# Performance work log

Hardware: AMD Instinct MI355X
Metric: run time of the kernel (lower is better)

## Reference

```python
import jax, jax.numpy as jnp
import numpy as np
import math

SAMPLE_RATIO = 0.25
K = 5
EPS = 1e-6

def _cells(loc_orig, H, W):
    # map normalized [-1,1] coords to nearest grid cell index, as in tcformer token2map/map2token
    loc = jnp.clip(loc_orig, -1.0, 1.0)
    px = jnp.clip(jnp.round(0.5 * (loc[..., 0] + 1.0) * W - 0.5).astype(jnp.int32), 0, W - 1)
    py = jnp.clip(jnp.round(0.5 * (loc[..., 1] + 1.0) * H - 0.5).astype(jnp.int32), 0, H - 1)
    return py * W + px  # [B, N0]

def token2map(x, loc_orig, idx_agg, H, W):
    B, N, C = x.shape
    N0 = loc_orig.shape[1]
    cell = _cells(loc_orig, H, W)
    seg = (cell + jnp.arange(B)[:, None] * (H * W)).reshape(-1)
    feat = x[jnp.arange(B)[:, None], idx_agg]  # [B, N0, C] token feature per original point
    sums = jax.ops.segment_sum(feat.reshape(-1, C), seg, num_segments=B * H * W)
    cnt = jax.ops.segment_sum(jnp.ones((B * N0,), x.dtype), seg, num_segments=B * H * W)
    x_map = sums / (cnt[:, None] + EPS)  # per-cell mean over points hitting the cell
    return x_map.reshape(B, H, W, C).transpose(0, 3, 1, 2)

def map2token(x_map, N, loc_orig, idx_agg, agg_weight):
    B, C, H, W = x_map.shape
    cell = _cells(loc_orig, H, W)
    val = x_map.reshape(B, C, H * W).transpose(0, 2, 1)  # [B, HW, C]
    vpt = val[jnp.arange(B)[:, None], cell]              # [B, N0, C] map value at each point
    seg = (idx_agg + jnp.arange(B)[:, None] * N).reshape(-1)
    w = agg_weight.reshape(-1)
    wsum = jax.ops.segment_sum(w, seg, num_segments=B * N) + EPS
    ssum = jax.ops.segment_sum(vpt.reshape(-1, C) * w[:, None], seg, num_segments=B * N)
    return (ssum / wsum[:, None]).reshape(B, N, C)  # agg_weight-weighted mean per token

def token_cluster_merge(x, Ns, idx_agg, weight, k):
    B, N, C = x.shape
    # DPC-KNN clustering (index computation; mirrors torch.no_grad block)
    sq = jnp.sum(x * x, -1)
    d2 = jnp.clip(sq[:, :, None] + sq[:, None, :] - 2.0 * jnp.einsum('bnc,bmc->bnm', x, x), 0.0, None)
    dist = jnp.sqrt(d2) / (C ** 0.5)
    dnear = -jax.lax.top_k(-dist, k)[0]                  # k smallest distances (incl. self)
    density = jnp.exp(-jnp.mean(dnear * dnear, -1))
    mask = density[:, None, :] > density[:, :, None]
    dmax = jnp.max(dist.reshape(B, -1), -1)[:, None, None]
    parent_dist = jnp.min(jnp.where(mask, dist, dmax), -1)  # dist to nearest higher-density token
    score = parent_dist * density
    index_down = jax.lax.top_k(score, Ns)[1]             # [B, Ns] cluster centers
    idx_cluster = jnp.argmin(dist[jnp.arange(B)[:, None], index_down], axis=1)  # [B, N]
    idx_cluster = idx_cluster.at[jnp.arange(B)[:, None], index_down].set(jnp.arange(Ns)[None, :])
    # weighted merge of tokens into clusters
    seg = (idx_cluster + jnp.arange(B)[:, None] * Ns).reshape(-1)
    w = weight.reshape(-1)
    allw = jax.ops.segment_sum(w, seg, num_segments=B * Ns) + EPS
    norm_w = (w / allw[seg]).reshape(B, N)
    x_merged = jax.ops.segment_sum((x * norm_w[:, :, None]).reshape(-1, C), seg, num_segments=B * Ns).reshape(B, Ns, C)
    idx_agg_down = idx_cluster[jnp.arange(B)[:, None], idx_agg]      # compose index maps
    weight_t = norm_w[jnp.arange(B)[:, None], idx_agg][..., None]    # [B, N0, 1]
    return x_merged, idx_agg_down, weight_t

def _forward(x, loc_orig, idx_agg, agg_weight, idx_k_loc, H, W, conv_w, conv_b, skip_w, ln_g, ln_b, conf_w, conf_b):
    B, N, C = x.shape
    x_map = token2map(x, loc_orig, idx_agg, H, W)
    x_map = jax.lax.conv_general_dilated(x_map, conv_w, (2, 2), ((1, 1), (1, 1))) + conv_b[None, :, None, None]
    x_tok = map2token(x_map, N, loc_orig, idx_agg, agg_weight) + jnp.einsum('bnc,oc->bno', x, skip_w)
    mu = jnp.mean(x_tok, -1, keepdims=True)
    var = jnp.mean((x_tok - mu) ** 2, -1, keepdims=True)
    x_tok = (x_tok - mu) / jnp.sqrt(var + 1e-5) * ln_g + ln_b
    conf = jnp.einsum('bnc,oc->bno', x_tok, conf_w) + conf_b
    weight = jnp.exp(conf)
    Ns = max(math.ceil(N * SAMPLE_RATIO), 1)
    x_down, idx_agg_down, weight_t = token_cluster_merge(x_tok, Ns, idx_agg, weight, K)
    agg_weight_down = agg_weight * weight_t
    agg_weight_down = agg_weight_down / jnp.max(agg_weight_down, axis=1, keepdims=True)
    # down_block is an injected submodule; treated as identity passthrough here
    return x_down, idx_agg_down, agg_weight_down

def setup_inputs():
    key = jax.random.key(0)
    ks = jax.random.split(key, 8)
    B, N, C, N0, Cout = 8, 256, 256, 16384, 512
    return {
        'x': jax.random.normal(ks[0], (B, N, C), jnp.float32),
        'loc_orig': jax.random.uniform(ks[1], (B, N0, 2), jnp.float32, -1.0, 1.0),
        'idx_agg': jax.random.randint(ks[2], (B, N0), 0, N),
        'agg_weight': jax.random.uniform(ks[3], (B, N0, 1), jnp.float32, 0.1, 1.0),
        'idx_k_loc': jax.random.randint(ks[4], (B, N0, K), 0, N0),
        'H': 64, 'W': 64,
        'conv_w': jax.random.normal(ks[5], (Cout, C, 3, 3), jnp.float32) * 0.02,
        'conv_b': jnp.zeros((Cout,), jnp.float32),
        'skip_w': jax.random.normal(ks[6], (Cout, C), jnp.float32) * 0.02,
        'ln_g': jnp.ones((Cout,), jnp.float32),
        'ln_b': jnp.zeros((Cout,), jnp.float32),
        'conf_w': jax.random.normal(ks[7], (1, Cout), jnp.float32) * 0.02,
        'conf_b': jnp.zeros((1,), jnp.float32),
    }

def reference(x, loc_orig, idx_agg, agg_weight, idx_k_loc, H, W, conv_w, conv_b, skip_w, ln_g, ln_b, conf_w, conf_b):
    return _forward(x, loc_orig, idx_agg, agg_weight, idx_k_loc, H, W, conv_w, conv_b, skip_w, ln_g, ln_b, conf_w, conf_b)
```

## Files before the change

kernel.cpp:

```cpp
#include <hip/hip_runtime.h>
#include <math.h>

typedef unsigned long long ull;
typedef __attribute__((ext_vector_type(8))) short short8v;
typedef __attribute__((ext_vector_type(4))) float float4v;

#define NB   8
#define NTOK 256
#define CIN  256
#define NP   16384
#define NCO  512
#define HW64 4096
#define OHW  1024
#define NS   64
#define EPS  1e-6f
#define KC   2304
#define NKC  72
#define KSPL 36

constexpr size_t OFF_SUMS = 0;
constexpr size_t OFF_CNT  = OFF_SUMS + (size_t)NB*HW64*CIN;
constexpr size_t OFF_AMAT = OFF_CNT  + (size_t)NB*HW64;
constexpr size_t OFF_ALLW = OFF_AMAT + (size_t)NB*NTOK*OHW;
constexpr size_t OFF_DMAX = OFF_ALLW + (size_t)NB*NS;
constexpr size_t OFF_MAXW = OFF_DMAX + NB;
constexpr size_t ZERO_END = OFF_MAXW + NB;
constexpr size_t OFF_WT   = ZERO_END;
constexpr size_t OFF_SKWT = OFF_WT   + (size_t)KC*NCO;
constexpr size_t OFF_Y    = OFF_SKWT + (size_t)CIN*NCO;
constexpr size_t OFF_C2   = OFF_Y    + (size_t)NB*OHW*NCO;
constexpr size_t OFF_WSUM = OFF_C2   + (size_t)NB*NTOK*NCO;
constexpr size_t OFF_XSKIP= OFF_WSUM + (size_t)NB*NTOK;
constexpr size_t OFF_XTOK = OFF_XSKIP+ (size_t)NB*NTOK*NCO;
constexpr size_t OFF_XPK  = OFF_XTOK + (size_t)NB*NTOK*NCO;
constexpr size_t OFF_WEXP = OFF_XPK  + (size_t)NB*NTOK*NCO;
constexpr size_t OFF_SQ   = OFF_WEXP + (size_t)NB*NTOK;
constexpr size_t OFF_DIST = OFF_SQ   + (size_t)NB*NTOK;
constexpr size_t OFF_DENS = OFF_DIST + (size_t)NB*NTOK*NTOK;
constexpr size_t OFF_SCORE= OFF_DENS + (size_t)NB*NTOK;
constexpr size_t OFF_IND  = OFF_SCORE+ (size_t)NB*NTOK;
constexpr size_t OFF_IDXCL= OFF_IND  + (size_t)NB*NS;
constexpr size_t OFF_NORMW= OFF_IDXCL+ (size_t)NB*NTOK;
constexpr size_t OFF_AWBUF= OFF_NORMW+ (size_t)NB*NTOK;
constexpr size_t OFF_XTPK = OFF_AWBUF+ (size_t)NB*NP;
constexpr size_t OFF_AMATP2= OFF_XTPK + (size_t)NB*CIN*NTOK;
constexpr size_t OFF_YPF1 = OFF_AMATP2+ (size_t)NB*NTOK*OHW;
constexpr size_t OFF_XTOKPK= OFF_Y;

__device__ __forceinline__ unsigned pack_hl(float x) {
    unsigned u = __float_as_uint(x);
    unsigned t = u + 0x7fffu + ((u >> 16) & 1u);
    unsigned hibits = t & 0xffff0000u;
    float lo = x - __uint_as_float(hibits);
    unsigned ul = __float_as_uint(lo);
    unsigned lt = ul + 0x7fffu + ((ul >> 16) & 1u);
    return hibits | (lt >> 16);
}
__device__ __forceinline__ unsigned hp2(unsigned w0, unsigned w1) {
    return __builtin_amdgcn_perm(w1, w0, 0x07060302u);
}
__device__ __forceinline__ unsigned lp2(unsigned w0, unsigned w1) {
    return __builtin_amdgcn_perm(w1, w0, 0x05040100u);
}

__global__ void hist(const float* __restrict__ loc, const int* __restrict__ idxagg,
                     const float* __restrict__ aggw,
                     int* __restrict__ cntmat, float* __restrict__ cnt,
                     float* __restrict__ amat) {
    int bp = blockIdx.x*256 + threadIdx.x;
    int b  = bp >> 14;
    float lx = loc[2*bp+0], ly = loc[2*bp+1];
    lx = fminf(fmaxf(lx, -1.f), 1.f);
    ly = fminf(fmaxf(ly, -1.f), 1.f);
    int px = (int)rintf((lx + 1.f)*32.f - 0.5f); px = min(max(px,0),63);
    int py = (int)rintf((ly + 1.f)*32.f - 0.5f); py = min(max(py,0),63);
    int cell = py*64 + px;
    int tok = idxagg[bp];
    atomicAdd(&cntmat[((size_t)(b*HW64 + cell))*NTOK + tok], 1);
    atomicAdd(&cnt[b*HW64 + cell], 1.0f);
    int qx = (int)rintf((lx + 1.f)*16.f - 0.5f); qx = min(max(qx,0),31);
    int qy = (int)rintf((ly + 1.f)*16.f - 0.5f); qy = min(max(qy,0),31);
    atomicAdd(&amat[((size_t)(b*NTOK + tok))*OHW + qy*32 + qx], aggw[bp]);
}

__global__ void cnt_pack(unsigned* __restrict__ m) {
    size_t i = (size_t)blockIdx.x*256 + threadIdx.x;
    int4 v = ((const int4*)m)[i];
    uint4 o;
    o.x = pack_hl((float)v.x); o.y = pack_hl((float)v.y);
    o.z = pack_hl((float)v.z); o.w = pack_hl((float)v.w);
    ((uint4*)m)[i] = o;
}

__global__ void xt_pack(const float* __restrict__ x, unsigned* __restrict__ xtpk) {
    int id = blockIdx.x*256 + threadIdx.x;
    int tok = id & 255, cin = (id >> 8) & 255, b = id >> 16;
    xtpk[id] = pack_hl(x[((size_t)(b*NTOK + tok))*CIN + cin]);
}

__global__ void wtrans(const float* __restrict__ convw, uint4* __restrict__ wtf) {
    int tid = blockIdx.x*256 + threadIdx.x;
    int lane = tid & 63;
    int r1 = tid >> 6;
    int h = r1 & 1;
    int r2 = r1 >> 1;
    int f = r2 & 3;
    int r3 = r2 >> 2;
    int kc = r3 % NKC, mt = r3 / NKC;
    int cout = mt*64 + f*16 + (lane & 15);
    int kb = kc*32 + (lane >> 4)*8;
    unsigned s[8];
    #pragma unroll
    for (int j = 0; j < 8; ++j) {
        int k = kb + j;
        int grp = k >> 8, cin = k & 255;
        unsigned w = pack_hl(convw[(size_t)cout*KC + cin*9 + grp]);
        s[j] = h ? (w & 0xffffu) : (w >> 16);
    }
    uint4 o;
    o.x = s[0] | (s[1]<<16); o.y = s[2] | (s[3]<<16);
    o.z = s[4] | (s[5]<<16); o.w = s[6] | (s[7]<<16);
    wtf[tid] = o;
}

__global__ void pack4(const float4* __restrict__ src, uint4* __restrict__ dst) {
    size_t i = (size_t)blockIdx.x*256 + threadIdx.x;
    float4 v = src[i];
    uint4 o;
    o.x = pack_hl(v.x); o.y = pack_hl(v.y); o.z = pack_hl(v.z); o.w = pack_hl(v.w);
    dst[i] = o;
}

__launch_bounds__(512)
__global__ void map_gemm(const unsigned* __restrict__ A, const unsigned* __restrict__ B,
                         const float* __restrict__ cnt, unsigned* __restrict__ xmapu) {
    __shared__ __align__(16) unsigned short Ah[4096];
    __shared__ __align__(16) unsigned short Bh[8192], Bl[8192];
    int z = blockIdx.z, m0 = blockIdx.y*128;
    const unsigned* Ab = A + ((size_t)z*HW64 + m0)*NTOK;
    const unsigned* Bb = B + (size_t)z*CIN*NTOK;
    int t = threadIdx.x, lane = t & 63;
    int w = t >> 6;
    int wm = w >> 2, wn = w & 3;
    int l15 = lane & 15, l4 = lane >> 4;
    int rowA = t & 127, kgA = t >> 7;
    int rowB = t & 255, kgB0 = (t >> 8)*2;
    const unsigned* arow = Ab + (size_t)rowA*NTOK + kgA*8;
    const unsigned* brow = Bb + (size_t)rowB*NTOK + kgB0*8;
    int wbA = (rowA>>4)*512 + kgA*128 + (rowA&15)*8;
    int wbB = (rowB>>4)*512 + kgB0*128 + (rowB&15)*8;

    float4v acc[4][4] = {};
    uint4 ra0, ra1, rb[2][2];
    auto loadA = [&](int kc) {
        const unsigned* p = arow + kc*32;
        ra0 = *(const uint4*)p; ra1 = *(const uint4*)(p + 4);
    };
    auto loadB = [&](int kc) {
        #pragma unroll
        for (int s = 0; s < 2; ++s) {
            const unsigned* p = brow + kc*32 + s*8;
            rb[s][0] = *(const uint4*)p; rb[s][1] = *(const uint4*)(p + 4);
        }
    };
    loadA(0); loadB(0);

    for (int kc = 0; kc < 8; ++kc) {
        __syncthreads();
        uint4 h, l;
        h.x=hp2(ra0.x,ra0.y); h.y=hp2(ra0.z,ra0.w); h.z=hp2(ra1.x,ra1.y); h.w=hp2(ra1.z,ra1.w);
        *(uint4*)&Ah[wbA] = h;
        #pragma unroll
        for (int s = 0; s < 2; ++s) {
            uint4 u0 = rb[s][0], u1 = rb[s][1];
            h.x=hp2(u0.x,u0.y); h.y=hp2(u0.z,u0.w); h.z=hp2(u1.x,u1.y); h.w=hp2(u1.z,u1.w);
            l.x=lp2(u0.x,u0.y); l.y=lp2(u0.z,u0.w); l.z=lp2(u1.x,u1.y); l.w=lp2(u1.z,u1.w);
            *(uint4*)&Bh[wbB + s*128] = h; *(uint4*)&Bl[wbB + s*128] = l;
        }
        __syncthreads();
        if (kc < 7) { loadA(kc+1); loadB(kc+1); }

        short8v bh[4], bl[4];
        #pragma unroll
        for (int q = 0; q < 4; ++q) {
            int off = (wn*4 + q)*512 + l4*128 + l15*8;
            bh[q] = *(const short8v*)&Bh[off];
            bl[q] = *(const short8v*)&Bl[off];
        }
        #pragma unroll
        for (int p = 0; p < 4; ++p) {
            int off = (wm*4 + p)*512 + l4*128 + l15*8;
            short8v ah = *(const short8v*)&Ah[off];
            #pragma unroll
            for (int q = 0; q < 4; ++q) {
                acc[p][q] = __builtin_amdgcn_mfma_f32_16x16x32_bf16(ah, bh[q], acc[p][q], 0, 0, 0);
                acc[p][q] = __builtin_amdgcn_mfma_f32_16x16x32_bf16(ah, bl[q], acc[p][q], 0, 0, 0);
            }
        }
    }

    const float* cntb = cnt + (size_t)z*HW64;
    #pragma unroll
    for (int p = 0; p < 4; ++p) {
        int mb = m0 + wm*64 + p*16 + l4*4;
        #pragma unroll
        for (int q = 0; q < 4; ++q) {
            int n = wn*64 + q*16 + l15;
            #pragma unroll
            for (int r = 0; r < 4; ++r) {
                float v = acc[p][q][r] / (cntb[mb + r] + EPS);
                xmapu[((size_t)z*HW64 + mb + r)*CIN + n] = pack_hl(v);
            }
        }
    }
}

__launch_bounds__(256)
__global__ void conv_gemm(const unsigned* __restrict__ xmap, const uint4* __restrict__ wtf,
                          float* __restrict__ yp0, float* __restrict__ yp1) {
    __shared__ __align__(16) unsigned short Ahi[2][4096], Alo[2][4096];
    int n0 = blockIdx.x * 128;
    int mt = blockIdx.y;
    int zsp = blockIdx.z;
    int kc0 = zsp * KSPL;
    int m0 = mt * 64;
    int t = threadIdx.x;
    int lane = t & 63, wid = t >> 6;
    int wm = wid >> 1, wn = wid & 1;
    int l15 = lane & 15, l4 = lane >> 4;

    int rowL = t & 127, kg = t >> 7;
    int posG = n0 + rowL;
    int bb = posG >> 10, rem = posG & 1023;
    int oy = rem >> 5, ox = rem & 31;

    int wbA0 = (rowL>>4)*512 + kg*128 + (rowL&15)*8;
    int wbA1 = wbA0 + 256;

    float4v acc[4][2] = {};
    uint4 a00,a01,a10,a11;

    auto loadA = [&](int kc) {
        int grp = kc >> 3;
        int ky = grp/3, kx = grp - 3*ky;
        int iy = 2*oy - 1 + ky, ix = 2*ox - 1 + kx;
        if ((unsigned)iy < 64u && (unsigned)ix < 64u) {
            const unsigned* ap = xmap + ((((size_t)bb*64 + iy)*64 + ix)*256 + (kc&7)*32 + kg*8);
            a00 = *(const uint4*)ap;       a01 = *(const uint4*)(ap + 4);
            a10 = *(const uint4*)(ap + 16); a11 = *(const uint4*)(ap + 20);
        } else {
            a00 = make_uint4(0,0,0,0); a01 = a00; a10 = a00; a11 = a00;
        }
    };
    auto repackA = [&](int buf) {
        uint4 h, l;
        h.x=hp2(a00.x,a00.y); h.y=hp2(a00.z,a00.w); h.z=hp2(a01.x,a01.y); h.w=hp2(a01.z,a01.w);
        l.x=lp2(a00.x,a00.y); l.y=lp2(a00.z,a00.w); l.z=lp2(a01.x,a01.y); l.w=lp2(a01.z,a01.w);
        *(uint4*)&Ahi[buf][wbA0] = h; *(uint4*)&Alo[buf][wbA0] = l;
        h.x=hp2(a10.x,a10.y); h.y=hp2(a10.z,a10.w); h.z=hp2(a11.x,a11.y); h.w=hp2(a11.z,a11.w);
        l.x=lp2(a10.x,a10.y); l.y=lp2(a10.z,a10.w); l.z=lp2(a11.x,a11.y); l.w=lp2(a11.z,a11.w);
        *(uint4*)&Ahi[buf][wbA1] = h; *(uint4*)&Alo[buf][wbA1] = l;
    };
    const uint4* wbase = wtf + ((size_t)(((mt*NKC)*4 + wn*2)*2))*64 + lane;

    short8v bhc[2], blc[2], bhn[2], bln[2];
    #pragma unroll
    for (int q = 0; q < 2; ++q) {
        bhc[q] = *(const short8v*)(wbase + (size_t)kc0*512 + q*128);
        blc[q] = *(const short8v*)(wbase + (size_t)kc0*512 + q*128 + 64);
    }
    loadA(kc0);
    repackA(0);
    __syncthreads();
    int cur = 0;

    for (int it = 0; it < KSPL; ++it) {
        int kc = kc0 + it;
        bool nl = (it + 1 < KSPL);
        if (nl) {
            loadA(kc+1);
            const uint4* wb = wbase + (size_t)(kc+1)*512;
            #pragma unroll
            for (int q = 0; q < 2; ++q) {
                bhn[q] = *(const short8v*)(wb + q*128);
                bln[q] = *(const short8v*)(wb + q*128 + 64);
            }
        }
        #pragma unroll
        for (int p = 0; p < 4; ++p) {
            int off = (wm*4 + p)*512 + l4*128 + l15*8;
            short8v ah = *(const short8v*)&Ahi[cur][off];
            short8v al = *(const short8v*)&Alo[cur][off];
            #pragma unroll
            for (int q = 0; q < 2; ++q) {
                acc[p][q] = __builtin_amdgcn_mfma_f32_16x16x32_bf16(ah, bhc[q], acc[p][q], 0, 0, 0);
                acc[p][q] = __builtin_amdgcn_mfma_f32_16x16x32_bf16(ah, blc[q], acc[p][q], 0, 0, 0);
                acc[p][q] = __builtin_amdgcn_mfma_f32_16x16x32_bf16(al, bhc[q], acc[p][q], 0, 0, 0);
            }
        }
        if (nl) {
            repackA(cur ^ 1);
            #pragma unroll
            for (int q = 0; q < 2; ++q) { bhc[q] = bhn[q]; blc[q] = bln[q]; }
        }
        __syncthreads();
        cur ^= 1;
    }

    float* yp = (zsp == 0) ? yp0 : yp1;
    int bbk = n0 >> 10;
    int pos0 = (n0 & 1023) + wm*64;
    #pragma unroll
    for (int p = 0; p < 4; ++p) {
        int posb = pos0 + p*16 + l4*4;
        #pragma unroll
        for (int q = 0; q < 2; ++q) {
            int col = m0 + wn*32 + q*16 + l15;
            *(float4v*)&yp[((size_t)(bbk*NCO + col))*OHW + posb] = acc[p][q];
        }
    }
}

__global__ void y_reduce(const float4* __restrict__ p0, const float4* __restrict__ p1,
                         const float* __restrict__ convb, uint4* __restrict__ out) {
    size_t i = (size_t)blockIdx.x*256 + threadIdx.x;
    int col = (int)((i >> 8) & 511);
    float bv = convb[col];
    float4 a = p0[i], b = p1[i];
    uint4 o;
    o.x = pack_hl(a.x + b.x + bv);
    o.y = pack_hl(a.y + b.y + bv);
    o.z = pack_hl(a.z + b.z + bv);
    o.w = pack_hl(a.w + b.w + bv);
    out[i] = o;
}

template<int MODE, int TM, int TN>
__launch_bounds__(256)
__global__ void gemm_pk(const unsigned* __restrict__ A, const unsigned* __restrict__ B,
                        float* __restrict__ C, int K, int N,
                        long sA, long sB, long sC,
                        const float* __restrict__ aux, unsigned* __restrict__ dmaxU) {
    constexpr int NA = TM/64, NBs = TN/64;
    constexpr int WSM = TM/64;
    constexpr int WSN = 4/WSM;
    constexpr int TWM = TM/WSM, TWN = TN/WSN;
    constexpr int P = TWM/16, Q = TWN/16;
    __shared__ __align__(16) unsigned short Ahi[TM*32], Alo[TM*32];
    __shared__ __align__(16) unsigned short Bhi[TN*32], Blo[TN*32];
    int z = blockIdx.z;
    const unsigned* Ab = A + (size_t)z*sA;
    const unsigned* Bb = B + (size_t)z*sB;
    float* Cb = C + (size_t)z*sC;
    int n0 = blockIdx.x*TN, m0 = blockIdx.y*TM;
    int t = threadIdx.x;
    int lane = t & 63, wid = t >> 6;
    int wm = (WSM==2) ? (wid >> 1) : 0;
    int wn = (WSM==2) ? (wid & 1)  : wid;
    int l15 = lane & 15, l4 = lane >> 4;

    int rowA = t & (TM-1), kgA = t / TM;
    int rowB = t & (TN-1), kgB = t / TN;
    const unsigned* arow = Ab + (size_t)(m0 + rowA)*K + kgA*8;
    const unsigned* brw  = Bb + (size_t)(n0 + rowB)*K + kgB*8;
    int wbA = (rowA>>4)*512 + kgA*128 + (rowA&15)*8;
    int wbB = (rowB>>4)*512 + kgB*128 + (rowB&15)*8;

    float4v acc[P][Q] = {};
    uint4 ra[NA][2], rb[NBs][2];
    auto loadA = [&](int kc) {
        #pragma unroll
        for (int s = 0; s < NA; ++s) {
            const unsigned* p = arow + (size_t)kc*32 + s*16;
            ra[s][0] = *(const uint4*)p; ra[s][1] = *(const uint4*)(p + 4);
        }
    };
    auto loadB = [&](int kc) {
        #pragma unroll
        for (int s = 0; s < NBs; ++s) {
            const unsigned* p = brw + (size_t)kc*32 + s*16;
            rb[s][0] = *(const uint4*)p; rb[s][1] = *(const uint4*)(p + 4);
        }
    };
    loadA(0); loadB(0);
    int nkc = K >> 5;

    for (int kc = 0; kc < nkc; ++kc) {
        __syncthreads();
        uint4 h, l;
        #pragma unroll
        for (int s = 0; s < NA; ++s) {
            uint4 u0 = ra[s][0], u1 = ra[s][1];
            h.x=hp2(u0.x,u0.y); h.y=hp2(u0.z,u0.w); h.z=hp2(u1.x,u1.y); h.w=hp2(u1.z,u1.w);
            l.x=lp2(u0.x,u0.y); l.y=lp2(u0.z,u0.w); l.z=lp2(u1.x,u1.y); l.w=lp2(u1.z,u1.w);
            *(uint4*)&Ahi[wbA + s*256] = h; *(uint4*)&Alo[wbA + s*256] = l;
        }
        #pragma unroll
        for (int s = 0; s < NBs; ++s) {
            uint4 u0 = rb[s][0], u1 = rb[s][1];
            h.x=hp2(u0.x,u0.y); h.y=hp2(u0.z,u0.w); h.z=hp2(u1.x,u1.y); h.w=hp2(u1.z,u1.w);
            l.x=lp2(u0.x,u0.y); l.y=lp2(u0.z,u0.w); l.z=lp2(u1.x,u1.y); l.w=lp2(u1.z,u1.w);
            *(uint4*)&Bhi[wbB + s*256] = h; *(uint4*)&Blo[wbB + s*256] = l;
        }
        __syncthreads();
        if (kc + 1 < nkc) { loadA(kc+1); loadB(kc+1); }

        short8v bh[Q], bl[Q];
        #pragma unroll
        for (int q = 0; q < Q; ++q) {
            int off = (wn*Q + q)*512 + l4*128 + l15*8;
            bh[q] = *(const short8v*)&Bhi[off];
            bl[q] = *(const short8v*)&Blo[off];
        }
        #pragma unroll
        for (int p = 0; p < P; ++p) {
            int off = (wm*P + p)*512 + l4*128 + l15*8;
            short8v ah = *(const short8v*)&Ahi[off];
            short8v al = *(const short8v*)&Alo[off];
            #pragma unroll
            for (int q = 0; q < Q; ++q) {
                acc[p][q] = __builtin_amdgcn_mfma_f32_16x16x32_bf16(ah, bh[q], acc[p][q], 0, 0, 0);
                acc[p][q] = __builtin_amdgcn_mfma_f32_16x16x32_bf16(ah, bl[q], acc[p][q], 0, 0, 0);
                acc[p][q] = __builtin_amdgcn_mfma_f32_16x16x32_bf16(al, bh[q], acc[p][q], 0, 0, 0);
            }
        }
    }

    if (MODE == 0) {
        #pragma unroll
        for (int p = 0; p < P; ++p) {
            int mb = m0 + wm*TWM + p*16 + l4*4;
            #pragma unroll
            for (int q = 0; q < Q; ++q) {
                int n = n0 + wn*TWN + q*16 + l15;
                #pragma unroll
                for (int r = 0; r < 4; ++r)
                    Cb[(size_t)(mb + r)*N + n] = acc[p][q][r];
            }
        }
    } else {
        const float inv = 1.0f / sqrtf(512.0f);
        const float* sqb = aux + (size_t)z*NTOK;
        float tmax = 0.f;
        #pragma unroll
        for (int p = 0; p < P; ++p) {
            int mb = m0 + wm*TWM + p*16 + l4*4;
            #pragma unroll
            for (int q = 0; q < Q; ++q) {
                int n = n0 + wn*TWN + q*16 + l15;
                float sn = sqb[n];
                #pragma unroll
                for (int r = 0; r < 4; ++r) {
                    float d2 = sqb[mb + r] + sn - 2.0f*acc[p][q][r];
                    float d = sqrtf(fmaxf(d2, 0.0f)) * inv;
                    Cb[(size_t)(mb + r)*N + n] = d;
                    tmax = fmaxf(tmax, d);
                }
            }
        }
        __shared__ float redm[4];
        #pragma unroll
        for (int off = 32; off; off >>= 1) tmax = fmaxf(tmax, __shfl_xor(tmax, off, 64));
        if (lane == 0) redm[wid] = tmax;
        __syncthreads();
        if (t == 0) {
            float m = fmaxf(fmaxf(redm[0], redm[1]), fmaxf(redm[2], redm[3]));
            atomicMax(dmaxU + z, __float_as_uint(m));
        }
    }
}

__global__ void wsum_rows(const float* __restrict__ amat, float* __restrict__ wsum) {
    int row = blockIdx.x*4 + (threadIdx.x >> 6);
    int lane = threadIdx.x & 63;
    const float* ar = amat + (size_t)row*OHW;
    float s = 0.f;
    #pragma unroll
    for (int r = 0; r < 16; ++r) s += ar[lane + 64*r];
    #pragma unroll
    for (int off = 32; off; off >>= 1) s += __shfl_xor(s, off, 64);
    if (lane == 0) wsum[row] = s;
}

__device__ __forceinline__ float block_sum256(float v, float* red) {
    #pragma unroll
    for (int off = 32; off; off >>= 1) v += __shfl_xor(v, off, 64);
    __syncthreads();
    if ((threadIdx.x & 63) == 0) red[threadIdx.x >> 6] = v;
    __syncthreads();
    return red[0] + red[1] + red[2] + red[3];
}

__global__ void ln_conf(const float* __restrict__ C2, const float* __restrict__ wsum,
                        const float* __restrict__ xskip, const float* __restrict__ g,
                        const float* __restrict__ be, const float* __restrict__ confw,
                        const float* __restrict__ confb, float* __restrict__ xtok,
                        unsigned* __restrict__ xtokpk,
                        float* __restrict__ wexp, float* __restrict__ sqv) {
    __shared__ float red[4];
    int row = blockIdx.x, t = threadIdx.x;
    float ws = wsum[row] + EPS;
    size_t base = (size_t)row*NCO;
    float v0 = C2[base + t]       / ws + xskip[base + t];
    float v1 = C2[base + t + 256] / ws + xskip[base + t + 256];
    float mu  = block_sum256(v0 + v1, red) / 512.0f;
    float d0 = v0 - mu, d1 = v1 - mu;
    float var = block_sum256(d0*d0 + d1*d1, red) / 512.0f;
    float sv = sqrtf(var + 1e-5f);
    float x0 = d0/sv * g[t]       + be[t];
    float x1 = d1/sv * g[t + 256] + be[t + 256];
    xtok[base + t] = x0;
    xtok[base + t + 256] = x1;
    xtokpk[base + t] = pack_hl(x0);
    xtokpk[base + t + 256] = pack_hl(x1);
    float cs = block_sum256(x0*confw[t] + x1*confw[t + 256], red);
    float qs = block_sum256(x0*x0 + x1*x1, red);
    if (t == 0) {
        wexp[row] = expf(cs + confb[0]);
        sqv[row]  = qs;
    }
}

__global__ void knn_dens(const float* __restrict__ dist, float* __restrict__ dens) {
    int row = blockIdx.x*4 + (threadIdx.x >> 6);
    int lane = threadIdx.x & 63;
    const float* dr = dist + (size_t)row*NTOK;
    float v0 = dr[lane], v1 = dr[lane+64], v2 = dr[lane+128], v3 = dr[lane+192];
    float acc = 0.f;
    #pragma unroll
    for (int it = 0; it < 5; ++it) {
        float lm = fminf(fminf(v0, v1), fminf(v2, v3));
        float gm = lm;
        #pragma unroll
        for (int off = 32; off; off >>= 1) gm = fminf(gm, __shfl_xor(gm, off, 64));
        acc += gm*gm;
        ull ball = __ballot(lm == gm);
        int first = __ffsll(ball) - 1;
        if (lane == first) {
            if      (v0 == gm) v0 = 1e30f;
            else if (v1 == gm) v1 = 1e30f;
            else if (v2 == gm) v2 = 1e30f;
            else               v3 = 1e30f;
        }
    }
    if (lane == 0) dens[row] = expf(-(acc/5.0f));
}

__global__ void parent_score(const float* __restrict__ dist, const float* __restrict__ dens,
                             const unsigned* __restrict__ dmaxU, float* __restrict__ score) {
    int row = blockIdx.x*4 + (threadIdx.x >> 6);
    int lane = threadIdx.x & 63;
    int b = row >> 8;
    float di = dens[row];
    float dm = __uint_as_float(dmaxU[b]);
    const float* dr = dist + (size_t)row*NTOK;
    const float* db = dens + (size_t)b*NTOK;
    float pd = dm;
    #pragma unroll
    for (int r = 0; r < 4; ++r) {
        int j = lane + 64*r;
        pd = fminf(pd, (db[j] > di) ? dr[j] : dm);
    }
    #pragma unroll
    for (int off = 32; off; off >>= 1) pd = fminf(pd, __shfl_xor(pd, off, 64));
    if (lane == 0) score[row] = pd * di;
}

__global__ void topk64(const float* __restrict__ score, int* __restrict__ ind) {
    int b = blockIdx.x, lane = threadIdx.x;
    const float* sb = score + b*NTOK;
    ull k0, k1, k2, k3;
    {
        unsigned i0 = lane, i1 = lane+64, i2 = lane+128, i3 = lane+192;
        k0 = ((ull)(__float_as_uint(sb[i0]) + 1u) << 32) | (unsigned)(4095 - i0);
        k1 = ((ull)(__float_as_uint(sb[i1]) + 1u) << 32) | (unsigned)(4095 - i1);
        k2 = ((ull)(__float_as_uint(sb[i2]) + 1u) << 32) | (unsigned)(4095 - i2);
        k3 = ((ull)(__float_as_uint(sb[i3]) + 1u) << 32) | (unsigned)(4095 - i3);
    }
    for (int it = 0; it < 64; ++it) {
        ull lm = k0;
        if (k1 > lm) lm = k1;
        if (k2 > lm) lm = k2;
        if (k3 > lm) lm = k3;
        ull gm = lm;
        #pragma unroll
        for (int off = 32; off; off >>= 1) {
            ull o = __shfl_xor(gm, off, 64);
            if (o > gm) gm = o;
        }
        if (lane == 0) ind[b*NS + it] = 4095 - (int)(gm & 0xffffffffull);
        if      (k0 == gm) k0 = 0;
        else if (k1 == gm) k1 = 0;
        else if (k2 == gm) k2 = 0;
        else if (k3 == gm) k3 = 0;
    }
}

__global__ void assign_k(const float* __restrict__ dist, const int* __restrict__ ind,
                         int* __restrict__ idxcl) {
    int row = blockIdx.x*4 + (threadIdx.x >> 6);
    int lane = threadIdx.x & 63;
    int b = row >> 8, i = row & 255;
    int center = ind[b*NS + lane];
    float d = dist[((size_t)(b*NTOK + center))*NTOK + i];
    ull key = ((ull)__float_as_uint(d) << 32) | (unsigned)lane;
    #pragma unroll
    for (int off = 32; off; off >>= 1) {
        ull o = __shfl_xor(key, off, 64);
        if (o < key) key = o;
    }
    if (lane == 0) idxcl[row] = (int)(key & 0xffffffffull);
}

__global__ void center_set(const int* __restrict__ ind, int* __restrict__ idxcl) {
    int id = threadIdx.x;
    int b = id >> 6, s = id & 63;
    idxcl[b*NTOK + ind[id]] = s;
}

__global__ void allw_acc(const int* __restrict__ idxcl, const float* __restrict__ wexp,
                         float* __restrict__ allw) {
    int b = blockIdx.x, i = threadIdx.x;
    atomicAdd(&allw[b*NS + idxcl[b*NTOK + i]], wexp[b*NTOK + i]);
}

__global__ void normw_k(const int* __restrict__ idxcl, const float* __restrict__ wexp,
                        const float* __restrict__ allw, float* __restrict__ normw) {
    int b = blockIdx.x, i = threadIdx.x;
    normw[b*NTOK + i] = wexp[b*NTOK + i] / (allw[b*NS + idxcl[b*NTOK + i]] + EPS);
}

__global__ void merge_k(const float* __restrict__ xtok, const int* __restrict__ idxcl,
                        const float* __restrict__ normw, float* __restrict__ xout) {
    int row = blockIdx.x, t = threadIdx.x;
    int b = row >> 8;
    int cl = idxcl[row];
    float nw = normw[row];
    float* o = xout + ((size_t)(b*NS + cl))*NCO;
    const float* xr = xtok + (size_t)row*NCO;
    atomicAdd(&o[t],       xr[t]       * nw);
    atomicAdd(&o[t + 256], xr[t + 256] * nw);
}

__global__ void out_idx_aw(const int* __restrict__ idxagg, const float* __restrict__ aggw,
                           const int* __restrict__ idxcl, const float* __restrict__ normw,
                           float* __restrict__ dout, float* __restrict__ awbuf,
                           unsigned* __restrict__ maxw) {
    __shared__ float red[4];
    int bp = blockIdx.x*256 + threadIdx.x;
    int b = bp >> 14;
    int tok = idxagg[bp];
    int cl = idxcl[b*NTOK + tok];
    dout[(size_t)NB*NS*NCO + bp] = (float)cl;
    float aw = aggw[bp] * normw[b*NTOK + tok];
    awbuf[bp] = aw;
    float m = aw;
    #pragma unroll
    for (int off = 32; off; off >>= 1) m = fmaxf(m, __shfl_xor(m, off, 64));
    if ((threadIdx.x & 63) == 0) red[threadIdx.x >> 6] = m;
    __syncthreads();
    if (threadIdx.x == 0) {
        float mm = fmaxf(fmaxf(red[0], red[1]), fmaxf(red[2], red[3]));
        atomicMax(&maxw[b], __float_as_uint(mm));
    }
}

__global__ void aw_final(const float* __restrict__ awbuf, const float* __restrict__ maxw,
                         float* __restrict__ dout) {
    int bp = blockIdx.x*256 + threadIdx.x;
    int b = bp >> 14;
    dout[(size_t)NB*NS*NCO + (size_t)NB*NP + bp] = awbuf[bp] / maxw[b];
}

extern "C" void kernel_launch(void* const* d_in, const int* in_sizes, int n_in,
                              void* d_out, int out_size, void* d_ws, size_t ws_size,
                              hipStream_t stream) {
    const float* x      = (const float*)d_in[0];
    const float* loc    = (const float*)d_in[1];
    const int*   idxagg = (const int*)  d_in[2];
    const float* aggw   = (const float*)d_in[3];
    const float* convw  = (const float*)d_in[7];
    const float* convb  = (const float*)d_in[8];
    const float* skipw  = (const float*)d_in[9];
    const float* lng    = (const float*)d_in[10];
    const float* lnb    = (const float*)d_in[11];
    const float* confw  = (const float*)d_in[12];
    const float* confb  = (const float*)d_in[13];

    float* ws = (float*)d_ws;
    float* dout = (float*)d_out;

    (void)hipMemsetAsync(ws, 0, ZERO_END*sizeof(float), stream);
    (void)hipMemsetAsync(dout, 0, (size_t)NB*NS*NCO*sizeof(float), stream);

    hist<<<dim3(NB*NP/256), 256, 0, stream>>>(loc, idxagg, aggw,
                                              (int*)(ws + OFF_SUMS), ws + OFF_CNT, ws + OFF_AMAT);
    cnt_pack<<<dim3(NB*HW64*CIN/1024), 256, 0, stream>>>((unsigned*)(ws + OFF_SUMS));
    xt_pack<<<dim3(NB*CIN*NTOK/256), 256, 0, stream>>>(x, (unsigned*)(ws + OFF_XTPK));
    wtrans<<<dim3(1152), 256, 0, stream>>>(convw, (uint4*)(ws + OFF_WT));
    pack4<<<dim3(CIN*NCO/1024), 256, 0, stream>>>((const float4*)skipw, (uint4*)(ws + OFF_SKWT));
    pack4<<<dim3(NB*NTOK*CIN/1024), 256, 0, stream>>>((const float4*)x, (uint4*)(ws + OFF_XPK));

    map_gemm<<<dim3(1, 32, 8), 512, 0, stream>>>((const unsigned*)(ws + OFF_SUMS),
                                                 (const unsigned*)(ws + OFF_XTPK),
                                                 ws + OFF_CNT,
                                                 (unsigned*)(ws + OFF_SUMS));

    conv_gemm<<<dim3(64, 8, 2), 256, 0, stream>>>((const unsigned*)(ws + OFF_SUMS),
                                                  (const uint4*)(ws + OFF_WT),
                                                  ws + OFF_Y, ws + OFF_YPF1);
    y_reduce<<<dim3(4096), 256, 0, stream>>>((const float4*)(ws + OFF_Y),
                                             (const float4*)(ws + OFF_YPF1),
                                             convb, (uint4*)(ws + OFF_Y));

    wsum_rows<<<dim3(NB*NTOK/4), 256, 0, stream>>>(ws + OFF_AMAT, ws + OFF_WSUM);
    pack4<<<dim3(NB*NTOK*OHW/1024), 256, 0, stream>>>((const float4*)(ws + OFF_AMAT),
                                                      (uint4*)(ws + OFF_AMATP2));
    gemm_pk<0,64,64><<<dim3(8, 4, 8), 256, 0, stream>>>((const unsigned*)(ws + OFF_AMATP2),
                                                  (const unsigned*)(ws + OFF_Y),
                                                  ws + OFF_C2, OHW, NCO,
                                                  (long)NTOK*OHW, (long)NCO*OHW, (long)NTOK*NCO,
                                                  nullptr, nullptr);
    gemm_pk<0,64,64><<<dim3(8, 32, 1), 256, 0, stream>>>((const unsigned*)(ws + OFF_XPK),
                                                   (const unsigned*)(ws + OFF_SKWT),
                                                   ws + OFF_XSKIP, CIN, NCO, 0, 0, 0,
                                                   nullptr, nullptr);

    ln_conf<<<dim3(NB*NTOK), 256, 0, stream>>>(ws + OFF_C2, ws + OFF_WSUM, ws + OFF_XSKIP,
                                               lng, lnb, confw, confb,
                                               ws + OFF_XTOK, (unsigned*)(ws + OFF_XTOKPK),
                                               ws + OFF_WEXP, ws + OFF_SQ);

    gemm_pk<1,64,64><<<dim3(4, 4, 8), 256, 0, stream>>>((const unsigned*)(ws + OFF_XTOKPK),
                                                  (const unsigned*)(ws + OFF_XTOKPK),
                                                  ws + OFF_DIST, NCO, NTOK,
                                                  (long)NTOK*NCO, (long)NTOK*NCO, (long)NTOK*NTOK,
                                                  ws + OFF_SQ, (unsigned*)(ws + OFF_DMAX));

    knn_dens<<<dim3(NB*NTOK/4), 256, 0, stream>>>(ws + OFF_DIST, ws + OFF_DENS);
    parent_score<<<dim3(NB*NTOK/4), 256, 0, stream>>>(ws + OFF_DIST, ws + OFF_DENS,
                                                      (const unsigned*)(ws + OFF_DMAX), ws + OFF_SCORE);
    topk64<<<dim3(NB), 64, 0, stream>>>(ws + OFF_SCORE, (int*)(ws + OFF_IND));
    assign_k<<<dim3(NB*NTOK/4), 256, 0, stream>>>(ws + OFF_DIST, (const int*)(ws + OFF_IND),
                                                  (int*)(ws + OFF_IDXCL));
    center_set<<<dim3(1), 512, 0, stream>>>((const int*)(ws + OFF_IND), (int*)(ws + OFF_IDXCL));
    allw_acc<<<dim3(NB), 256, 0, stream>>>((const int*)(ws + OFF_IDXCL), ws + OFF_WEXP, ws + OFF_ALLW);
    normw_k<<<dim3(NB), 256, 0, stream>>>((const int*)(ws + OFF_IDXCL), ws + OFF_WEXP,
                                          ws + OFF_ALLW, ws + OFF_NORMW);
    merge_k<<<dim3(NB*NTOK), 256, 0, stream>>>(ws + OFF_XTOK, (const int*)(ws + OFF_IDXCL),
                                               ws + OFF_NORMW, dout);
    out_idx_aw<<<dim3(NB*NP/256), 256, 0, stream>>>(idxagg, aggw, (const int*)(ws + OFF_IDXCL),
                                                    ws + OFF_NORMW, dout, ws + OFF_AWBUF,
                                                    (unsigned*)(ws + OFF_MAXW));
    aw_final<<<dim3(NB*NP/256), 256, 0, stream>>>(ws + OFF_AWBUF, (const float*)(ws + OFF_MAXW), dout);
}
```

Measured before the change: 315.7 us.

## Fuse pack passes into GEMM loaders and drop conv split-K reduction

Removes the separate count-pack pass: map_gemm now reads raw int counts and converts them to bf16 in its loader. The amat pack pass is folded into gemm_pk through a new template flag that packs fp32 on load, and both x packings now come from a single kernel. conv_gemm no longer splits K into two halves; each block runs the full K loop and writes the biased, packed output directly, so y_reduce and the partial buffers go away. This saves several full-tensor read/write passes and launches, but conv_gemm now has half as many blocks (512), each with a K loop twice as long, which may reduce parallelism.

```diff
diff --git a/kernel.cpp b/kernel.cpp
--- a/kernel.cpp
+++ b/kernel.cpp
@@ -16,7 +16,6 @@
 #define EPS  1e-6f
 #define KC   2304
 #define NKC  72
-#define KSPL 36
 
 constexpr size_t OFF_SUMS = 0;
 constexpr size_t OFF_CNT  = OFF_SUMS + (size_t)NB*HW64*CIN;
@@ -43,8 +42,6 @@
 constexpr size_t OFF_NORMW= OFF_IDXCL+ (size_t)NB*NTOK;
 constexpr size_t OFF_AWBUF= OFF_NORMW+ (size_t)NB*NTOK;
 constexpr size_t OFF_XTPK = OFF_AWBUF+ (size_t)NB*NP;
-constexpr size_t OFF_AMATP2= OFF_XTPK + (size_t)NB*CIN*NTOK;
-constexpr size_t OFF_YPF1 = OFF_AMATP2+ (size_t)NB*NTOK*OHW;
 constexpr size_t OFF_XTOKPK= OFF_Y;
 
 __device__ __forceinline__ unsigned pack_hl(float x) {
@@ -55,6 +52,10 @@
     unsigned ul = __float_as_uint(lo);
     unsigned lt = ul + 0x7fffu + ((ul >> 16) & 1u);
     return hibits | (lt >> 16);
+}
+__device__ __forceinline__ unsigned f2bf(float f) {
+    unsigned u = __float_as_uint(f);
+    return (u + 0x7fffu + ((u >> 16) & 1u)) >> 16;
 }
 __device__ __forceinline__ unsigned hp2(unsigned w0, unsigned w1) {
     return __builtin_amdgcn_perm(w1, w0, 0x07060302u);
@@ -83,19 +84,13 @@
     atomicAdd(&amat[((size_t)(b*NTOK + tok))*OHW + qy*32 + qx], aggw[bp]);
 }
 
-__global__ void cnt_pack(unsigned* __restrict__ m) {
-    size_t i = (size_t)blockIdx.x*256 + threadIdx.x;
-    int4 v = ((const int4*)m)[i];
-    uint4 o;
-    o.x = pack_hl((float)v.x); o.y = pack_hl((float)v.y);
-    o.z = pack_hl((float)v.z); o.w = pack_hl((float)v.w);
-    ((uint4*)m)[i] = o;
-}
-
-__global__ void xt_pack(const float* __restrict__ x, unsigned* __restrict__ xtpk) {
+__global__ void xpack_both(const float* __restrict__ x, unsigned* __restrict__ xtpk,
+                           unsigned* __restrict__ xpk) {
     int id = blockIdx.x*256 + threadIdx.x;
     int tok = id & 255, cin = (id >> 8) & 255, b = id >> 16;
-    xtpk[id] = pack_hl(x[((size_t)(b*NTOK + tok))*CIN + cin]);
+    unsigned pk = pack_hl(x[((size_t)(b*NTOK + tok))*CIN + cin]);
+    xtpk[id] = pk;
+    xpk[((size_t)(b*NTOK + tok))*CIN + cin] = pk;
 }
 
 __global__ void wtrans(const float* __restrict__ convw, uint4* __restrict__ wtf) {
@@ -132,12 +127,12 @@
 }
 
 __launch_bounds__(512)
-__global__ void map_gemm(const unsigned* __restrict__ A, const unsigned* __restrict__ B,
+__global__ void map_gemm(const int* __restrict__ A, const unsigned* __restrict__ B,
                          const float* __restrict__ cnt, unsigned* __restrict__ xmapu) {
     __shared__ __align__(16) unsigned short Ah[4096];
     __shared__ __align__(16) unsigned short Bh[8192], Bl[8192];
     int z = blockIdx.z, m0 = blockIdx.y*128;
-    const unsigned* Ab = A + ((size_t)z*HW64 + m0)*NTOK;
+    const int* Ab = A + ((size_t)z*HW64 + m0)*NTOK;
     const unsigned* Bb = B + (size_t)z*CIN*NTOK;
     int t = threadIdx.x, lane = t & 63;
     int w = t >> 6;
@@ -145,16 +140,17 @@
     int l15 = lane & 15, l4 = lane >> 4;
     int rowA = t & 127, kgA = t >> 7;
     int rowB = t & 255, kgB0 = (t >> 8)*2;
-    const unsigned* arow = Ab + (size_t)rowA*NTOK + kgA*8;
+    const int* arow = Ab + (size_t)rowA*NTOK + kgA*8;
     const unsigned* brow = Bb + (size_t)rowB*NTOK + kgB0*8;
     int wbA = (rowA>>4)*512 + kgA*128 + (rowA&15)*8;
     int wbB = (rowB>>4)*512 + kgB0*128 + (rowB&15)*8;
 
     float4v acc[4][4] = {};
-    uint4 ra0, ra1, rb[2][2];
+    int4 ia0, ia1;
+    uint4 rb[2][2];
     auto loadA = [&](int kc) {
-        const unsigned* p = arow + kc*32;
-        ra0 = *(const uint4*)p; ra1 = *(const uint4*)(p + 4);
+        const int* p = arow + kc*32;
+        ia0 = *(const int4*)p; ia1 = *(const int4*)(p + 4);
     };
     auto loadB = [&](int kc) {
         #pragma unroll
@@ -168,7 +164,10 @@
     for (int kc = 0; kc < 8; ++kc) {
         __syncthreads();
         uint4 h, l;
-        h.x=hp2(ra0.x,ra0.y); h.y=hp2(ra0.z,ra0.w); h.z=hp2(ra1.x,ra1.y); h.w=hp2(ra1.z,ra1.w);
+        h.x = f2bf((float)ia0.x) | (f2bf((float)ia0.y) << 16);
+        h.y = f2bf((float)ia0.z) | (f2bf((float)ia0.w) << 16);
+        h.z = f2bf((float)ia1.x) | (f2bf((float)ia1.y) << 16);
+        h.w = f2bf((float)ia1.z) | (f2bf((float)ia1.w) << 16);
         *(uint4*)&Ah[wbA] = h;
         #pragma unroll
         for (int s = 0; s < 2; ++s) {
@@ -217,12 +216,12 @@
 
 __launch_bounds__(256)
 __global__ void conv_gemm(const unsigned* __restrict__ xmap, const uint4* __restrict__ wtf,
-                          float* __restrict__ yp0, float* __restrict__ yp1) {
+                          const float* __restrict__ convb, unsigned* __restrict__ ytp) {
     __shared__ __align__(16) unsigned short Ahi[2][4096], Alo[2][4096];
-    int n0 = blockIdx.x * 128;
-    int mt = blockIdx.y;
-    int zsp = blockIdx.z;
-    int kc0 = zsp * KSPL;
+    int bid = blockIdx.x;
+    int mt = bid & 7;
+    int xt = bid >> 3;
+    int n0 = xt * 128;
     int m0 = mt * 64;
     int t = threadIdx.x;
     int lane = t & 63, wid = t >> 6;
@@ -266,17 +265,16 @@
     short8v bhc[2], blc[2], bhn[2], bln[2];
     #pragma unroll
     for (int q = 0; q < 2; ++q) {
-        bhc[q] = *(const short8v*)(wbase + (size_t)kc0*512 + q*128);
-        blc[q] = *(const short8v*)(wbase + (size_t)kc0*512 + q*128 + 64);
-    }
-    loadA(kc0);
+        bhc[q] = *(const short8v*)(wbase + q*128);
+        blc[q] = *(const short8v*)(wbase + q*128 + 64);
+    }
+    loadA(0);
     repackA(0);
     __syncthreads();
     int cur = 0;
 
-    for (int it = 0; it < KSPL; ++it) {
-        int kc = kc0 + it;
-        bool nl = (it + 1 < KSPL);
+    for (int kc = 0; kc < NKC; ++kc) {
+        bool nl = (kc + 1 < NKC);
         if (nl) {
             loadA(kc+1);
             const uint4* wb = wbase + (size_t)(kc+1)*512;
@@ -307,7 +305,6 @@
         cur ^= 1;
     }
 
-    float* yp = (zsp == 0) ? yp0 : yp1;
     int bbk = n0 >> 10;
     int pos0 = (n0 & 1023) + wm*64;
     #pragma unroll
@@ -316,28 +313,20 @@
         #pragma unroll
         for (int q = 0; q < 2; ++q) {
             int col = m0 + wn*32 + q*16 + l15;
-            *(float4v*)&yp[((size_t)(bbk*NCO + col))*OHW + posb] = acc[p][q];
-        }
-    }
-}
-
-__global__ void y_reduce(const float4* __restrict__ p0, const float4* __restrict__ p1,
-                         const float* __restrict__ convb, uint4* __restrict__ out) {
-    size_t i = (size_t)blockIdx.x*256 + threadIdx.x;
-    int col = (int)((i >> 8) & 511);
-    float bv = convb[col];
-    float4 a = p0[i], b = p1[i];
-    uint4 o;
-    o.x = pack_hl(a.x + b.x + bv);
-    o.y = pack_hl(a.y + b.y + bv);
-    o.z = pack_hl(a.z + b.z + bv);
-    o.w = pack_hl(a.w + b.w + bv);
-    out[i] = o;
-}
-
-template<int MODE, int TM, int TN>
+            float bv = convb[col];
+            uint4 o;
+            o.x = pack_hl(acc[p][q][0] + bv);
+            o.y = pack_hl(acc[p][q][1] + bv);
+            o.z = pack_hl(acc[p][q][2] + bv);
+            o.w = pack_hl(acc[p][q][3] + bv);
+            *(uint4*)&ytp[((size_t)(bbk*NCO + col))*OHW + posb] = o;
+        }
+    }
+}
+
+template<int MODE, int TM, int TN, int AF>
 __launch_bounds__(256)
-__global__ void gemm_pk(const unsigned* __restrict__ A, const unsigned* __restrict__ B,
+__global__ void gemm_pk(const void* __restrict__ Av, const unsigned* __restrict__ B,
                         float* __restrict__ C, int K, int N,
                         long sA, long sB, long sC,
                         const float* __restrict__ aux, unsigned* __restrict__ dmaxU) {
@@ -349,7 +338,7 @@
     __shared__ __align__(16) unsigned short Ahi[TM*32], Alo[TM*32];
     __shared__ __align__(16) unsigned short Bhi[TN*32], Blo[TN*32];
     int z = blockIdx.z;
-    const unsigned* Ab = A + (size_t)z*sA;
+    const unsigned* Ab = (const unsigned*)Av + (size_t)z*sA;
     const unsigned* Bb = B + (size_t)z*sB;
     float* Cb = C + (size_t)z*sC;
     int n0 = blockIdx.x*TN, m0 = blockIdx.y*TM;
@@ -391,8 +380,19 @@
         #pragma unroll
         for (int s = 0; s < NA; ++s) {
             uint4 u0 = ra[s][0], u1 = ra[s][1];
-            h.x=hp2(u0.x,u0.y); h.y=hp2(u0.z,u0.w); h.z=hp2(u1.x,u1.y); h.w=hp2(u1.z,u1.w);
-            l.x=lp2(u0.x,u0.y); l.y=lp2(u0.z,u0.w); l.z=lp2(u1.x,u1.y); l.w=lp2(u1.z,u1.w);
+            if (AF == 0) {
+                h.x=hp2(u0.x,u0.y); h.y=hp2(u0.z,u0.w); h.z=hp2(u1.x,u1.y); h.w=hp2(u1.z,u1.w);
+                l.x=lp2(u0.x,u0.y); l.y=lp2(u0.z,u0.w); l.z=lp2(u1.x,u1.y); l.w=lp2(u1.z,u1.w);
+            } else {
+                unsigned pk0 = pack_hl(__uint_as_float(u0.x)), pk1 = pack_hl(__uint_as_float(u0.y));
+                unsigned pk2 = pack_hl(__uint_as_float(u0.z)), pk3 = pack_hl(__uint_as_float(u0.w));
+                unsigned pk4 = pack_hl(__uint_as_float(u1.x)), pk5 = pack_hl(__uint_as_float(u1.y));
+                unsigned pk6 = pack_hl(__uint_as_float(u1.z)), pk7 = pack_hl(__uint_as_float(u1.w));
+                h.x = (pk0>>16) | (pk1 & 0xffff0000u); h.y = (pk2>>16) | (pk3 & 0xffff0000u);
+                h.z = (pk4>>16) | (pk5 & 0xffff0000u); h.w = (pk6>>16) | (pk7 & 0xffff0000u);
+                l.x = (pk0&0xffffu) | (pk1<<16); l.y = (pk2&0xffffu) | (pk3<<16);
+                l.z = (pk4&0xffffu) | (pk5<<16); l.w = (pk6&0xffffu) | (pk7<<16);
+            }
             *(uint4*)&Ahi[wbA + s*256] = h; *(uint4*)&Alo[wbA + s*256] = l;
         }
         #pragma unroll
@@ -695,33 +695,27 @@
 
     hist<<<dim3(NB*NP/256), 256, 0, stream>>>(loc, idxagg, aggw,
                                               (int*)(ws + OFF_SUMS), ws + OFF_CNT, ws + OFF_AMAT);
-    cnt_pack<<<dim3(NB*HW64*CIN/1024), 256, 0, stream>>>((unsigned*)(ws + OFF_SUMS));
-    xt_pack<<<dim3(NB*CIN*NTOK/256), 256, 0, stream>>>(x, (unsigned*)(ws + OFF_XTPK));
+    xpack_both<<<dim3(NB*CIN*NTOK/256), 256, 0, stream>>>(x, (unsigned*)(ws + OFF_XTPK),
+                                                          (unsigned*)(ws + OFF_XPK));
     wtrans<<<dim3(1152), 256, 0, stream>>>(convw, (uint4*)(ws + OFF_WT));
     pack4<<<dim3(CIN*NCO/1024), 256, 0, stream>>>((const float4*)skipw, (uint4*)(ws + OFF_SKWT));
-    pack4<<<dim3(NB*NTOK*CIN/1024), 256, 0, stream>>>((const float4*)x, (uint4*)(ws + OFF_XPK));
-
-    map_gemm<<<dim3(1, 32, 8), 512, 0, stream>>>((const unsigned*)(ws + OFF_SUMS),
+
+    map_gemm<<<dim3(1, 32, 8), 512, 0, stream>>>((const int*)(ws + OFF_SUMS),
                                                  (const unsigned*)(ws + OFF_XTPK),
                                                  ws + OFF_CNT,
                                                  (unsigned*)(ws + OFF_SUMS));
 
-    conv_gemm<<<dim3(64, 8, 2), 256, 0, stream>>>((const unsigned*)(ws + OFF_SUMS),
-                                                  (const uint4*)(ws + OFF_WT),
-                                                  ws + OFF_Y, ws + OFF_YPF1);
-    y_reduce<<<dim3(4096), 256, 0, stream>>>((const float4*)(ws + OFF_Y),
-                                             (const float4*)(ws + OFF_YPF1),
-                                             convb, (uint4*)(ws + OFF_Y));
+    conv_gemm<<<dim3(512), 256, 0, stream>>>((const unsigned*)(ws + OFF_SUMS),
+                                             (const uint4*)(ws + OFF_WT), convb,
+                                             (unsigned*)(ws + OFF_Y));
 
     wsum_rows<<<dim3(NB*NTOK/4), 256, 0, stream>>>(ws + OFF_AMAT, ws + OFF_WSUM);
-    pack4<<<dim3(NB*NTOK*OHW/1024), 256, 0, stream>>>((const float4*)(ws + OFF_AMAT),
-                                                      (uint4*)(ws + OFF_AMATP2));
-    gemm_pk<0,64,64><<<dim3(8, 4, 8), 256, 0, stream>>>((const unsigned*)(ws + OFF_AMATP2),
+    gemm_pk<0,64,64,1><<<dim3(8, 4, 8), 256, 0, stream>>>((const void*)(ws + OFF_AMAT),
                                                   (const unsigned*)(ws + OFF_Y),
                                                   ws + OFF_C2, OHW, NCO,
                                                   (long)NTOK*OHW, (long)NCO*OHW, (long)NTOK*NCO,
                                                   nullptr, nullptr);
-    gemm_pk<0,64,64><<<dim3(8, 32, 1), 256, 0, stream>>>((const unsigned*)(ws + OFF_XPK),
+    gemm_pk<0,64,64,0><<<dim3(8, 32, 1), 256, 0, stream>>>((const void*)(ws + OFF_XPK),
                                                    (const unsigned*)(ws + OFF_SKWT),
                                                    ws + OFF_XSKIP, CIN, NCO, 0, 0, 0,
                                                    nullptr, nullptr);
@@ -731,7 +725,7 @@
                                                ws + OFF_XTOK, (unsigned*)(ws + OFF_XTOKPK),
                                                ws + OFF_WEXP, ws + OFF_SQ);
 
-    gemm_pk<1,64,64><<<dim3(4, 4, 8), 256, 0, stream>>>((const unsigned*)(ws + OFF_XTOKPK),
+    gemm_pk<1,64,64,0><<<dim3(4, 4, 8), 256, 0, stream>>>((const void*)(ws + OFF_XTOKPK),
                                                   (const unsigned*)(ws + OFF_XTOKPK),
                                                   ws + OFF_DIST, NCO, NTOK,
                                                   (long)NTOK*NCO, (long)NTOK*NCO, (long)NTOK*NTOK,
```

New measurement: 306.4 us. 3.0% less time.
